# Performance work log

Measured on AMD Instinct MI355X. Metric: run time of the kernel, lower is better.

Reference implementation:

```python
import jax, jax.numpy as jnp
import numpy as np

N_HEADS = 16
HIDDEN = 256
DIM = 4096
SEQ_LEN = 4096
BATCH = 8192
DECAY_CONSTANT = SEQ_LEN // 512  # = 8


def setup_inputs() -> dict:
    key = jax.random.key(0)
    ks = jax.random.split(key, 9)
    return {
        "x": jax.random.normal(ks[0], (BATCH, DIM), dtype=jnp.float32),
        "proj_w": jax.random.normal(ks[1], (N_HEADS, HIDDEN, DIM), dtype=jnp.float32) * 0.02,
        "proj_b": jax.random.normal(ks[2], (N_HEADS, HIDDEN), dtype=jnp.float32) * 0.02,
        "mix_w": jax.random.normal(ks[3], (N_HEADS, SEQ_LEN), dtype=jnp.float32) * 0.02 + 1.0,
        "mix_b": jax.random.normal(ks[4], (N_HEADS, SEQ_LEN), dtype=jnp.float32) * 0.02,
        "decay_value": jax.random.uniform(ks[5], (N_HEADS,), dtype=jnp.float32, minval=0.85, maxval=1.05),
        "cache": jax.random.normal(ks[6], (N_HEADS, BATCH, HIDDEN), dtype=jnp.float32),
        "out_w": jax.random.normal(ks[7], (DIM, DIM), dtype=jnp.float32) * 0.02,
        "out_b": jax.random.normal(ks[8], (DIM,), dtype=jnp.float32) * 0.02,
        "index": 1000,
    }


def reference(x, proj_w, proj_b, mix_w, mix_b, decay_value, cache, out_w, out_b, index):
    # Per-head projections: [h, b, k]
    proj = jnp.einsum("bd,hkd->hbk", x, proj_w) + proj_b[:, None, :]

    # Mixer params at the given sequence index (scalar per head)
    w = mix_w[:, index]          # [h]
    b = mix_b[:, index]          # [h]
    decay = jnp.clip(decay_value, 0.9, 1.0) ** (1.0 / DECAY_CONSTANT)  # [h]

    # First n_heads//2 heads are Col-style: out = w*x + w*decay*cache + b
    # Last  n_heads//2 heads are Row-style: out = w*x +   decay*cache + b
    is_col = jnp.arange(N_HEADS) < (N_HEADS // 2)
    cache_coef = jnp.where(is_col, w * decay, decay)  # [h]

    out = (w[:, None, None] * proj
           + cache_coef[:, None, None] * cache
           + b[:, None, None])  # [h, b, k]

    # Concatenate heads along feature axis -> [batch, n_heads*hidden] = [batch, dim]
    hidden = jnp.transpose(out, (1, 0, 2)).reshape(x.shape[0], N_HEADS * HIDDEN)

    return hidden @ out_w.T + out_b
```

## Files before the change

kernel.cpp:

```cpp
#include <hip/hip_runtime.h>
#include <hip/hip_bf16.h>

#define MROW 8192
#define DIMK 4096
#define NCOL 4096
#define HID  256
#define NH   16
#define SEQL 4096

#define BKT 32
#define NKT (DIMK / BKT)
#define SLOTB 32768
#define LDS_TOTAL (4 * SLOTB)

typedef __attribute__((ext_vector_type(8))) short short8;
typedef __attribute__((ext_vector_type(4))) float f32x4;

__device__ inline ushort f2bf(float f) {
  unsigned u = __float_as_uint(f);
  u += 0x7FFF + ((u >> 16) & 1);
  return (ushort)(u >> 16);
}

__device__ inline void gload16(const void* g, void* l) {
  __builtin_amdgcn_global_load_lds(
      (const __attribute__((address_space(1))) void*)g,
      (__attribute__((address_space(3))) void*)l, 16, 0, 0);
}

__global__ void cvt_f32_bf16(const float* __restrict__ s, ushort* __restrict__ d, long n8) {
  long stride = (long)gridDim.x * blockDim.x;
  for (long i = (long)blockIdx.x * blockDim.x + threadIdx.x; i < n8; i += stride) {
    const float4* s4 = (const float4*)(s + i * 8);
    float4 a = s4[0], b = s4[1];
    ushort r[8] = {f2bf(a.x), f2bf(a.y), f2bf(a.z), f2bf(a.w),
                   f2bf(b.x), f2bf(b.y), f2bf(b.z), f2bf(b.w)};
    *(uint4*)(d + i * 8) = *(const uint4*)r;
  }
}

__global__ void coef_kernel(const float* __restrict__ mix_w, const float* __restrict__ mix_b,
                            const float* __restrict__ decay_value, const float* __restrict__ proj_b,
                            const int* __restrict__ index_p,
                            float* __restrict__ wv, float* __restrict__ cc, float* __restrict__ pb2) {
  int n = blockIdx.x * blockDim.x + threadIdx.x;
  if (n >= NCOL) return;
  int h = n >> 8;
  int idx = *index_p;
  float w  = mix_w[h * SEQL + idx];
  float bb = mix_b[h * SEQL + idx];
  float dv = fminf(fmaxf(decay_value[h], 0.9f), 1.0f);
  float decay = powf(dv, 0.125f);
  float coef = (h < NH / 2) ? w * decay : decay;
  wv[n]  = w;
  cc[n]  = coef;
  pb2[n] = w * proj_b[n] + bb;
}

template <int EPI>
__global__ __launch_bounds__(512, 2) void gemmp(
    const ushort* __restrict__ A, const ushort* __restrict__ B,
    float* __restrict__ outf, ushort* __restrict__ outh,
    const float* __restrict__ cache, const float* __restrict__ wv,
    const float* __restrict__ cc, const float* __restrict__ pb2,
    const float* __restrict__ outb) {
  extern __shared__ __align__(16) char smem[];

  const int tid  = threadIdx.x;
  const int lane = tid & 63;
  const int wid  = tid >> 6;
  const int wr = wid >> 2;
  const int wc = wid & 3;
  const int r16 = lane & 15;
  const int cq  = lane >> 4;

  const int bid = blockIdx.x;
  const int swz = (bid & 7) * 64 + (bid >> 3);
  const int bm = swz >> 4, bn = swz & 15;
  const int m0 = bm * 256, n0 = bn * 256;

  const ushort* Ag = A + (size_t)m0 * DIMK;
  const ushort* Bg = B + (size_t)n0 * DIMK;

  int aoff[8], boff[4];
#pragma unroll
  for (int i = 0; i < 8; ++i) {
    int arow = wr * 128 + i * 16 + r16;
    aoff[i] = arow * 64 + ((cq ^ ((arow >> 1) & 3)) << 4);
  }
#pragma unroll
  for (int i = 0; i < 4; ++i) {
    int brow = wc * 64 + i * 16 + r16;
    boff[i] = 16384 + brow * 64 + ((cq ^ ((brow >> 1) & 3)) << 4);
  }

  int soff[2], sgo[2];
#pragma unroll
  for (int j = 0; j < 2; ++j) {
    int off = j * 8192 + tid * 16;
    int row = off >> 6;
    soff[j] = off;
    sgo[j]  = row * DIMK + ((((off >> 4) & 3) ^ ((row >> 1) & 3)) << 3);
  }

  f32x4 acc[8][4] = {};

#pragma unroll
  for (int kt = 0; kt < 3; ++kt) {
    char* s = smem + kt * SLOTB;
#pragma unroll
    for (int j = 0; j < 2; ++j) {
      gload16(Ag + (size_t)sgo[j] + kt * BKT, s + soff[j]);
      gload16(Bg + (size_t)sgo[j] + kt * BKT, s + 16384 + soff[j]);
    }
  }
  asm volatile("s_waitcnt vmcnt(4)" ::: "memory");
  __builtin_amdgcn_s_barrier();
  __builtin_amdgcn_sched_barrier(0);

  short8 blo[4], alo[4];
#pragma unroll
  for (int i = 0; i < 4; ++i) blo[i] = *(const short8*)(smem + boff[i]);
#pragma unroll
  for (int i = 0; i < 4; ++i) alo[i] = *(const short8*)(smem + aoff[i]);

  for (int kt = 0; kt < NKT; ++kt) {
    const char* cur = smem + (kt & 3) * SLOTB;
    const char* nxt = smem + ((kt + 1) & 3) * SLOTB;
    char*       st  = smem + ((kt + 3) & 3) * SLOTB;
    const bool  do_st = kt < NKT - 3;
    const int   k3 = (kt + 3) * BKT;

    short8 ahi[4];
#pragma unroll
    for (int i = 0; i < 4; ++i) ahi[i] = *(const short8*)(cur + aoff[4 + i]);
    if (do_st) {
      gload16(Ag + (size_t)sgo[0] + k3, st + soff[0]);
      gload16(Ag + (size_t)sgo[1] + k3, st + soff[1]);
    }
    __builtin_amdgcn_sched_barrier(0);
    __builtin_amdgcn_s_setprio(1);
#pragma unroll
    for (int mi = 0; mi < 4; ++mi)
#pragma unroll
      for (int ni = 0; ni < 4; ++ni)
        acc[mi][ni] = __builtin_amdgcn_mfma_f32_16x16x32_bf16(alo[mi], blo[ni], acc[mi][ni], 0, 0, 0);
    __builtin_amdgcn_s_setprio(0);

    short8 bn[4], an[4];
    if (kt < NKT - 1) {
#pragma unroll
      for (int i = 0; i < 4; ++i) bn[i] = *(const short8*)(nxt + boff[i]);
#pragma unroll
      for (int i = 0; i < 4; ++i) an[i] = *(const short8*)(nxt + aoff[i]);
    }
    if (do_st) {
      gload16(Bg + (size_t)sgo[0] + k3, st + 16384 + soff[0]);
      gload16(Bg + (size_t)sgo[1] + k3, st + 16384 + soff[1]);
    }
    __builtin_amdgcn_sched_barrier(0);
    __builtin_amdgcn_s_setprio(1);
#pragma unroll
    for (int mi = 0; mi < 4; ++mi)
#pragma unroll
      for (int ni = 0; ni < 4; ++ni)
        acc[4 + mi][ni] = __builtin_amdgcn_mfma_f32_16x16x32_bf16(ahi[mi], blo[ni], acc[4 + mi][ni], 0, 0, 0);
    __builtin_amdgcn_s_setprio(0);

    if (kt < NKT - 3)       asm volatile("s_waitcnt vmcnt(4)" ::: "memory");
    else if (kt == NKT - 3) asm volatile("s_waitcnt vmcnt(0)" ::: "memory");
    __builtin_amdgcn_s_barrier();
    __builtin_amdgcn_sched_barrier(0);

#pragma unroll
    for (int i = 0; i < 4; ++i) { blo[i] = bn[i]; alo[i] = an[i]; }
  }

  const int colb = n0 + wc * 64 + r16;
  const int rowb = m0 + wr * 128 + cq * 4;

  float wvv[4], ccv[4], pbv[4], obv[4];
#pragma unroll
  for (int ni = 0; ni < 4; ++ni) {
    int n = colb + ni * 16;
    if (EPI == 1) { wvv[ni] = wv[n]; ccv[ni] = cc[n]; pbv[ni] = pb2[n]; }
    else          { obv[ni] = outb[n]; }
  }

#pragma unroll
  for (int am = 0; am < 8; ++am) {
    int mrow = rowb + am * 16;
#pragma unroll
    for (int ni = 0; ni < 4; ++ni) {
      f32x4 v = acc[am][ni];
      int n = colb + ni * 16;
#pragma unroll
      for (int r = 0; r < 4; ++r) {
        int m = mrow + r;
        if (EPI == 1) {
          int h = n >> 8, kq = n & 255;
          float val = wvv[ni] * v[r] + ccv[ni] * cache[((size_t)h * MROW + m) * HID + kq] + pbv[ni];
          outh[(size_t)m * NCOL + n] = f2bf(val);
        } else {
          outf[(size_t)m * NCOL + n] = v[r] + obv[ni];
        }
      }
    }
  }
}

extern "C" void kernel_launch(void* const* d_in, const int* in_sizes, int n_in,
                              void* d_out, int out_size, void* d_ws, size_t ws_size,
                              hipStream_t stream) {
  const float* x      = (const float*)d_in[0];
  const float* proj_w = (const float*)d_in[1];
  const float* proj_b = (const float*)d_in[2];
  const float* mix_w  = (const float*)d_in[3];
  const float* mix_b  = (const float*)d_in[4];
  const float* decay  = (const float*)d_in[5];
  const float* cache  = (const float*)d_in[6];
  const float* out_w  = (const float*)d_in[7];
  const float* out_b  = (const float*)d_in[8];
  const int*   index  = (const int*)d_in[9];

  char* ws = (char*)d_ws;
  ushort* xb  = (ushort*)ws;
  ushort* pwb = (ushort*)(ws + 67108864);
  ushort* owb = (ushort*)(ws + 100663296);
  ushort* hid = (ushort*)(ws + 134217728);
  float*  wv  = (float*)(ws + 201326592);
  float*  cc  = (float*)(ws + 201326592 + 16384);
  float*  pb2 = (float*)(ws + 201326592 + 32768);

  hipFuncSetAttribute((const void*)&gemmp<1>, hipFuncAttributeMaxDynamicSharedMemorySize, LDS_TOTAL);
  hipFuncSetAttribute((const void*)&gemmp<0>, hipFuncAttributeMaxDynamicSharedMemorySize, LDS_TOTAL);

  hipLaunchKernelGGL(cvt_f32_bf16, dim3(2048), dim3(256), 0, stream,
                     x, xb, (long)MROW * DIMK / 8);
  hipLaunchKernelGGL(cvt_f32_bf16, dim3(1024), dim3(256), 0, stream,
                     proj_w, pwb, (long)NCOL * DIMK / 8);
  hipLaunchKernelGGL(cvt_f32_bf16, dim3(1024), dim3(256), 0, stream,
                     out_w, owb, (long)NCOL * DIMK / 8);
  hipLaunchKernelGGL(coef_kernel, dim3(16), dim3(256), 0, stream,
                     mix_w, mix_b, decay, proj_b, index, wv, cc, pb2);

  hipLaunchKernelGGL((gemmp<1>), dim3((MROW / 256) * (NCOL / 256)), dim3(512), LDS_TOTAL, stream,
                     xb, pwb, nullptr, hid, cache, wv, cc, pb2, nullptr);
  hipLaunchKernelGGL((gemmp<0>), dim3((MROW / 256) * (NCOL / 256)), dim3(512), LDS_TOTAL, stream,
                     hid, owb, (float*)d_out, nullptr, nullptr, nullptr, nullptr, nullptr, out_b);
}
```

Baseline: 599.3 us.

## Restructure GEMM main loop into 8-phase barrier-synchronized schedule

Replaces the register double-buffered K loop with a loop unrolled by two K-tiles, split into four phases per tile pair. Each phase loads LDS fragments, issues half of the global-to-LDS prefetch, and then runs a barrier plus lgkmcnt wait before a block of MFMAs. The goal is to interleave loads and MFMA issue across waves more regularly, in the style of the ping-pong 8-wave schedule. In exchange it adds many more workgroup barriers per iteration and drops the register prefetch of the next tile's fragments, so LDS latency is no longer hidden.

```diff
diff --git a/kernel.cpp b/kernel.cpp
--- a/kernel.cpp
+++ b/kernel.cpp
@@ -10,11 +10,15 @@
 
 #define BKT 32
 #define NKT (DIMK / BKT)
+#define NIT (NKT / 2)
 #define SLOTB 32768
 #define LDS_TOTAL (4 * SLOTB)
 
 typedef __attribute__((ext_vector_type(8))) short short8;
 typedef __attribute__((ext_vector_type(4))) float f32x4;
+
+#define BAR() __builtin_amdgcn_s_barrier()
+#define LG0() asm volatile("s_waitcnt lgkmcnt(0)" ::: "memory")
 
 __device__ inline ushort f2bf(float f) {
   unsigned u = __float_as_uint(f);
@@ -58,7 +62,7 @@
 }
 
 template <int EPI>
-__global__ __launch_bounds__(512, 2) void gemmp(
+__global__ __launch_bounds__(512, 2) void gemm8p(
     const ushort* __restrict__ A, const ushort* __restrict__ B,
     float* __restrict__ outf, ushort* __restrict__ outh,
     const float* __restrict__ cache, const float* __restrict__ wv,
@@ -82,16 +86,15 @@
   const ushort* Ag = A + (size_t)m0 * DIMK;
   const ushort* Bg = B + (size_t)n0 * DIMK;
 
-  int aoff[8], boff[4];
-#pragma unroll
-  for (int i = 0; i < 8; ++i) {
-    int arow = wr * 128 + i * 16 + r16;
-    aoff[i] = arow * 64 + ((cq ^ ((arow >> 1) & 3)) << 4);
-  }
+  int aoff0[4], aoff1[4], boff[4];
 #pragma unroll
   for (int i = 0; i < 4; ++i) {
-    int brow = wc * 64 + i * 16 + r16;
-    boff[i] = 16384 + brow * 64 + ((cq ^ ((brow >> 1) & 3)) << 4);
+    int r0 = wr * 128 + i * 16 + r16;
+    aoff0[i] = r0 * 64 + ((cq ^ ((r0 >> 1) & 3)) << 4);
+    int r1 = r0 + 64;
+    aoff1[i] = r1 * 64 + ((cq ^ ((r1 >> 1) & 3)) << 4);
+    int rb = wc * 64 + i * 16 + r16;
+    boff[i] = 16384 + rb * 64 + ((cq ^ ((rb >> 1) & 3)) << 4);
   }
 
   int soff[2], sgo[2];
@@ -109,71 +112,83 @@
   for (int kt = 0; kt < 3; ++kt) {
     char* s = smem + kt * SLOTB;
 #pragma unroll
-    for (int j = 0; j < 2; ++j) {
-      gload16(Ag + (size_t)sgo[j] + kt * BKT, s + soff[j]);
-      gload16(Bg + (size_t)sgo[j] + kt * BKT, s + 16384 + soff[j]);
-    }
-  }
-  asm volatile("s_waitcnt vmcnt(4)" ::: "memory");
-  __builtin_amdgcn_s_barrier();
-  __builtin_amdgcn_sched_barrier(0);
-
-  short8 blo[4], alo[4];
-#pragma unroll
-  for (int i = 0; i < 4; ++i) blo[i] = *(const short8*)(smem + boff[i]);
-#pragma unroll
-  for (int i = 0; i < 4; ++i) alo[i] = *(const short8*)(smem + aoff[i]);
-
-  for (int kt = 0; kt < NKT; ++kt) {
-    const char* cur = smem + (kt & 3) * SLOTB;
-    const char* nxt = smem + ((kt + 1) & 3) * SLOTB;
-    char*       st  = smem + ((kt + 3) & 3) * SLOTB;
-    const bool  do_st = kt < NKT - 3;
-    const int   k3 = (kt + 3) * BKT;
-
-    short8 ahi[4];
-#pragma unroll
-    for (int i = 0; i < 4; ++i) ahi[i] = *(const short8*)(cur + aoff[4 + i]);
-    if (do_st) {
-      gload16(Ag + (size_t)sgo[0] + k3, st + soff[0]);
-      gload16(Ag + (size_t)sgo[1] + k3, st + soff[1]);
-    }
-    __builtin_amdgcn_sched_barrier(0);
-    __builtin_amdgcn_s_setprio(1);
-#pragma unroll
-    for (int mi = 0; mi < 4; ++mi)
-#pragma unroll
-      for (int ni = 0; ni < 4; ++ni)
-        acc[mi][ni] = __builtin_amdgcn_mfma_f32_16x16x32_bf16(alo[mi], blo[ni], acc[mi][ni], 0, 0, 0);
-    __builtin_amdgcn_s_setprio(0);
-
-    short8 bn[4], an[4];
-    if (kt < NKT - 1) {
-#pragma unroll
-      for (int i = 0; i < 4; ++i) bn[i] = *(const short8*)(nxt + boff[i]);
-#pragma unroll
-      for (int i = 0; i < 4; ++i) an[i] = *(const short8*)(nxt + aoff[i]);
-    }
-    if (do_st) {
-      gload16(Bg + (size_t)sgo[0] + k3, st + 16384 + soff[0]);
-      gload16(Bg + (size_t)sgo[1] + k3, st + 16384 + soff[1]);
-    }
-    __builtin_amdgcn_sched_barrier(0);
-    __builtin_amdgcn_s_setprio(1);
-#pragma unroll
-    for (int mi = 0; mi < 4; ++mi)
-#pragma unroll
-      for (int ni = 0; ni < 4; ++ni)
-        acc[4 + mi][ni] = __builtin_amdgcn_mfma_f32_16x16x32_bf16(ahi[mi], blo[ni], acc[4 + mi][ni], 0, 0, 0);
-    __builtin_amdgcn_s_setprio(0);
-
-    if (kt < NKT - 3)       asm volatile("s_waitcnt vmcnt(4)" ::: "memory");
-    else if (kt == NKT - 3) asm volatile("s_waitcnt vmcnt(0)" ::: "memory");
-    __builtin_amdgcn_s_barrier();
-    __builtin_amdgcn_sched_barrier(0);
-
-#pragma unroll
-    for (int i = 0; i < 4; ++i) { blo[i] = bn[i]; alo[i] = an[i]; }
+    for (int j = 0; j < 2; ++j) gload16(Ag + (size_t)sgo[j] + kt * BKT, s + soff[j]);
+#pragma unroll
+    for (int j = 0; j < 2; ++j) gload16(Bg + (size_t)sgo[j] + kt * BKT, s + 16384 + soff[j]);
+  }
+  asm volatile("s_waitcnt vmcnt(8)" ::: "memory");
+  BAR();
+
+  for (int it = 0; it < NIT; ++it) {
+    const int kt = it * 2;
+    const char* s0 = smem + (kt & 3) * SLOTB;
+    const char* s1 = smem + ((kt + 1) & 3) * SLOTB;
+    char* st1 = smem + ((kt + 3) & 3) * SLOTB;
+    char* st2 = smem + (kt & 3) * SLOTB;
+    const bool do1 = (kt + 3) < NKT, do2 = (kt + 4) < NKT;
+    const size_t k1 = (size_t)(kt + 3) * BKT, k2 = (size_t)(kt + 4) * BKT;
+
+    short8 af[4], bf[4];
+
+#pragma unroll
+    for (int i = 0; i < 4; ++i) bf[i] = *(const short8*)(s0 + boff[i]);
+#pragma unroll
+    for (int i = 0; i < 4; ++i) af[i] = *(const short8*)(s0 + aoff0[i]);
+    if (do1) { gload16(Ag + sgo[0] + k1, st1 + soff[0]); gload16(Ag + sgo[1] + k1, st1 + soff[1]); }
+    BAR(); LG0();
+    __builtin_amdgcn_s_setprio(1);
+#pragma unroll
+    for (int mi = 0; mi < 4; ++mi)
+#pragma unroll
+      for (int ni = 0; ni < 4; ++ni)
+        acc[mi][ni] = __builtin_amdgcn_mfma_f32_16x16x32_bf16(af[mi], bf[ni], acc[mi][ni], 0, 0, 0);
+    __builtin_amdgcn_s_setprio(0);
+    BAR();
+
+#pragma unroll
+    for (int i = 0; i < 4; ++i) af[i] = *(const short8*)(s0 + aoff1[i]);
+    if (do1) { gload16(Bg + sgo[0] + k1, st1 + 16384 + soff[0]); gload16(Bg + sgo[1] + k1, st1 + 16384 + soff[1]); }
+    BAR(); LG0();
+    __builtin_amdgcn_s_setprio(1);
+#pragma unroll
+    for (int mi = 0; mi < 4; ++mi)
+#pragma unroll
+      for (int ni = 0; ni < 4; ++ni)
+        acc[4 + mi][ni] = __builtin_amdgcn_mfma_f32_16x16x32_bf16(af[mi], bf[ni], acc[4 + mi][ni], 0, 0, 0);
+    __builtin_amdgcn_s_setprio(0);
+    if (it < NIT - 1) asm volatile("s_waitcnt vmcnt(8)" ::: "memory");
+    else              asm volatile("s_waitcnt vmcnt(0)" ::: "memory");
+    BAR();
+
+#pragma unroll
+    for (int i = 0; i < 4; ++i) bf[i] = *(const short8*)(s1 + boff[i]);
+#pragma unroll
+    for (int i = 0; i < 4; ++i) af[i] = *(const short8*)(s1 + aoff0[i]);
+    if (do2) { gload16(Ag + sgo[0] + k2, st2 + soff[0]); gload16(Ag + sgo[1] + k2, st2 + soff[1]); }
+    BAR(); LG0();
+    __builtin_amdgcn_s_setprio(1);
+#pragma unroll
+    for (int mi = 0; mi < 4; ++mi)
+#pragma unroll
+      for (int ni = 0; ni < 4; ++ni)
+        acc[mi][ni] = __builtin_amdgcn_mfma_f32_16x16x32_bf16(af[mi], bf[ni], acc[mi][ni], 0, 0, 0);
+    __builtin_amdgcn_s_setprio(0);
+    BAR();
+
+#pragma unroll
+    for (int i = 0; i < 4; ++i) af[i] = *(const short8*)(s1 + aoff1[i]);
+    if (do2) { gload16(Bg + sgo[0] + k2, st2 + 16384 + soff[0]); gload16(Bg + sgo[1] + k2, st2 + 16384 + soff[1]); }
+    BAR(); LG0();
+    __builtin_amdgcn_s_setprio(1);
+#pragma unroll
+    for (int mi = 0; mi < 4; ++mi)
+#pragma unroll
+      for (int ni = 0; ni < 4; ++ni)
+        acc[4 + mi][ni] = __builtin_amdgcn_mfma_f32_16x16x32_bf16(af[mi], bf[ni], acc[4 + mi][ni], 0, 0, 0);
+    __builtin_amdgcn_s_setprio(0);
+    if (it < NIT - 2)       asm volatile("s_waitcnt vmcnt(8)" ::: "memory");
+    else if (it == NIT - 2) asm volatile("s_waitcnt vmcnt(4)" ::: "memory");
+    BAR();
   }
 
   const int colb = n0 + wc * 64 + r16;
@@ -232,8 +247,8 @@
   float*  cc  = (float*)(ws + 201326592 + 16384);
   float*  pb2 = (float*)(ws + 201326592 + 32768);
 
-  hipFuncSetAttribute((const void*)&gemmp<1>, hipFuncAttributeMaxDynamicSharedMemorySize, LDS_TOTAL);
-  hipFuncSetAttribute((const void*)&gemmp<0>, hipFuncAttributeMaxDynamicSharedMemorySize, LDS_TOTAL);
+  hipFuncSetAttribute((const void*)&gemm8p<1>, hipFuncAttributeMaxDynamicSharedMemorySize, LDS_TOTAL);
+  hipFuncSetAttribute((const void*)&gemm8p<0>, hipFuncAttributeMaxDynamicSharedMemorySize, LDS_TOTAL);
 
   hipLaunchKernelGGL(cvt_f32_bf16, dim3(2048), dim3(256), 0, stream,
                      x, xb, (long)MROW * DIMK / 8);
@@ -244,8 +259,8 @@
   hipLaunchKernelGGL(coef_kernel, dim3(16), dim3(256), 0, stream,
                      mix_w, mix_b, decay, proj_b, index, wv, cc, pb2);
 
-  hipLaunchKernelGGL((gemmp<1>), dim3((MROW / 256) * (NCOL / 256)), dim3(512), LDS_TOTAL, stream,
+  hipLaunchKernelGGL((gemm8p<1>), dim3((MROW / 256) * (NCOL / 256)), dim3(512), LDS_TOTAL, stream,
                      xb, pwb, nullptr, hid, cache, wv, cc, pb2, nullptr);
-  hipLaunchKernelGGL((gemmp<0>), dim3((MROW / 256) * (NCOL / 256)), dim3(512), LDS_TOTAL, stream,
+  hipLaunchKernelGGL((gemm8p<0>), dim3((MROW / 256) * (NCOL / 256)), dim3(512), LDS_TOTAL, stream,
                      hid, owb, (float*)d_out, nullptr, nullptr, nullptr, nullptr, nullptr, out_b);
 }
```

Measured after the change: 591.0 us. Within noise of the previous version (-1.4%).
